# Optimization experiments

Hardware: AMD Instinct MI355X
Metric: run time of the kernel (lower is better)

Reference implementation:

```python
import jax, jax.numpy as jnp
import numpy as np

B, IN, H, O, T = 4096, 128, 1024, 64, 25  # batch, static feat, hidden, outputs, steps


def setup_inputs() -> dict:
    key = jax.random.key(0)
    ks = jax.random.split(key, 11)
    s = 1.0 / np.sqrt(H)  # PyTorch LSTM/Linear uniform init scale
    u = lambda k, sh: jax.random.uniform(k, sh, jnp.float32, -s, s)
    return {
        "static_input": jax.random.normal(ks[0], (B, IN), jnp.float32),
        "W_ih0": u(ks[1], (4 * H, IN + O)),
        "W_hh0": u(ks[2], (4 * H, H)),
        "b_ih0": u(ks[3], (4 * H,)),
        "b_hh0": u(ks[4], (4 * H,)),
        "W_ih1": u(ks[5], (4 * H, H)),
        "W_hh1": u(ks[6], (4 * H, H)),
        "b_ih1": u(ks[7], (4 * H,)),
        "b_hh1": u(ks[8], (4 * H,)),
        "W_out": u(ks[9], (O, H)),
        "b_out": u(ks[10], (O,)),
        "num_steps": T,
    }


def _lstm_cell(x, h, c, W_ih, W_hh, b):
    # PyTorch gate order: input, forget, cell(g), output
    g = x @ W_ih.T + h @ W_hh.T + b
    i, f, gg, o = jnp.split(g, 4, axis=-1)
    c_new = jax.nn.sigmoid(f) * c + jax.nn.sigmoid(i) * jnp.tanh(gg)
    h_new = jax.nn.sigmoid(o) * jnp.tanh(c_new)
    return h_new, c_new


def reference(static_input, W_ih0, W_hh0, b_ih0, b_hh0,
              W_ih1, W_hh1, b_ih1, b_hh1, W_out, b_out, num_steps):
    b0 = b_ih0 + b_hh0
    b1 = b_ih1 + b_hh1
    batch = static_input.shape[0]
    hid = W_hh0.shape[1]
    out_dim = W_out.shape[0]
    z = jnp.zeros((batch, hid), jnp.float32)
    y0 = jnp.zeros((batch, out_dim), jnp.float32)  # output_seq[:, 0] is zeros at t=0

    def step(carry, _):
        h1, c1, h2, c2, y_prev = carry
        x = jnp.concatenate([static_input, y_prev], axis=-1)  # [B, IN+O]
        h1, c1 = _lstm_cell(x, h1, c1, W_ih0, W_hh0, b0)
        h2, c2 = _lstm_cell(h1, h2, c2, W_ih1, W_hh1, b1)
        y = h2 @ W_out.T + b_out  # [B, O]
        return (h1, c1, h2, c2, y), y

    _, ys = jax.lax.scan(step, (z, z, z, z, y0), None, length=num_steps)
    return jnp.transpose(ys, (1, 0, 2))  # [B, T, O]
```

## Files before the change

### kernel.cpp

```cpp
#include <hip/hip_runtime.h>

#define BATCH  4096
#define HID    1024
#define NOUT   64
#define TSTEPS 25
#define KA2    1216
#define KB     2048
#define LDY    1600

typedef __attribute__((ext_vector_type(8))) __bf16 bf16x8;
typedef __attribute__((ext_vector_type(4))) float  floatx4;

__device__ __forceinline__ unsigned short f2bf(float f) {
    union { float f; unsigned u; } v; v.f = f;
    unsigned r = v.u + 0x7fffu + ((v.u >> 16) & 1u);
    return (unsigned short)(r >> 16);
}
__device__ __forceinline__ float rcpf(float x) { return __builtin_amdgcn_rcpf(x); }
__device__ __forceinline__ float sigmf(float x) { return rcpf(1.0f + __expf(-x)); }
__device__ __forceinline__ float tanh_fast(float x) {
    float ax = fabsf(x);
    float e  = __expf(-2.0f * ax);
    float t  = (1.0f - e) * rcpf(1.0f + e);
    return copysignf(t, x);
}

#define GLDS16(gp, lp) __builtin_amdgcn_global_load_lds( \
    (const __attribute__((address_space(1))) void*)(gp), \
    (__attribute__((address_space(3))) void*)(lp), 16, 0, 0)

__global__ __launch_bounds__(1024, 4) void lstm_gate_gemm(
    const unsigned short* __restrict__ X, int K,
    const unsigned short* __restrict__ W,
    const float* __restrict__ ginit,
    float* __restrict__ cell,
    unsigned short* __restrict__ d1, int ld1, int off1,
    unsigned short* __restrict__ d2, int ld2, int off2,
    float* __restrict__ dfp)
{
    __shared__ __align__(16) char smem[65536];

    const int tid  = threadIdx.x;
    const int lane = tid & 63;
    const int w    = tid >> 6;
    const int q    = lane >> 4;
    const int lr   = lane & 15;
    const int wm   = w >> 2;
    const int wn   = w & 3;

    const int id  = blockIdx.y * 16 + blockIdx.x;
    const int xcd = id & 7;
    const int c   = id >> 3;
    const int bx  = (xcd & 3) * 4 + (c & 3);
    const int by  = (xcd >> 2) * 8 + (c >> 2);
    const int m0  = bx * 256;
    const int j0  = by * 64;

    const unsigned short* srcS[2];
    char* ldsS[2];
#pragma unroll
    for (int e = 0; e < 2; ++e) {
        int s = e * 1024 + tid;
        if (s < 1024) {
            int row = s >> 2;
            int kg  = (s & 3) ^ ((row >> 1) & 3);
            srcS[e] = X + (size_t)(m0 + row) * K + kg * 8;
        } else {
            int t   = s - 1024;
            int row = t >> 2;
            int kg  = (t & 3) ^ ((row >> 1) & 3);
            int jj = row >> 2, gate = row & 3;
            srcS[e] = W + (size_t)(gate * HID + j0 + jj) * K + kg * 8;
        }
        ldsS[e] = smem + (size_t)s * 16;
    }

    unsigned offA[4], offB[4];
#pragma unroll
    for (int i = 0; i < 4; ++i) {
        int ra = wm * 64 + i * 16 + lr;
        offA[i] = (unsigned)((ra * 4 + (q ^ ((ra >> 1) & 3))) * 16);
        int rb = wn * 64 + i * 16 + lr;
        offB[i] = (unsigned)(16384 + (rb * 4 + (q ^ ((rb >> 1) & 3))) * 16);
    }

    floatx4 acc[4][4];
#pragma unroll
    for (int i = 0; i < 4; ++i)
#pragma unroll
        for (int j = 0; j < 4; ++j)
            acc[i][j] = floatx4{0.f, 0.f, 0.f, 0.f};

    const int kiters = K >> 5;

#pragma unroll
    for (int e = 0; e < 2; ++e)
        GLDS16(srcS[e], ldsS[e]);

    for (int kt = 0; kt < kiters; ++kt) {
        __syncthreads();
        const int cur = (kt & 1) * 32768;
        if (kt + 1 < kiters) {
            const int koff = (kt + 1) * 32;
            const int nxt  = ((kt + 1) & 1) * 32768;
#pragma unroll
            for (int e = 0; e < 2; ++e)
                GLDS16(srcS[e] + koff, ldsS[e] + nxt);
        }
        bf16x8 av[4], bv[4];
#pragma unroll
        for (int j = 0; j < 4; ++j) bv[j] = *(const bf16x8*)(smem + cur + offB[j]);
#pragma unroll
        for (int i = 0; i < 4; ++i) av[i] = *(const bf16x8*)(smem + cur + offA[i]);
#pragma unroll
        for (int i = 0; i < 4; ++i)
#pragma unroll
            for (int j = 0; j < 4; ++j)
                acc[i][j] = __builtin_amdgcn_mfma_f32_16x16x32_bf16(av[i], bv[j], acc[i][j], 0, 0, 0);
    }

    const int jg = j0 + wn * 16 + lr;
    const float4 gi = *(const float4*)(ginit + (size_t)jg * 4);
    float* scratch = (float*)(void*)smem + w * 1024;

#pragma unroll
    for (int i = 0; i < 4; ++i) {
        __syncthreads();
#pragma unroll
        for (int j = 0; j < 4; ++j)
#pragma unroll
            for (int r = 0; r < 4; ++r)
                scratch[(q * 4 + r) * 64 + j * 16 + lr] = acc[i][j][r];
        __syncthreads();
#pragma unroll
        for (int p = 0; p < 4; ++p) {
            int row = q + p * 4;
            const float4 g = *(const float4*)(scratch + row * 64 + lr * 4);
            int b = m0 + wm * 64 + i * 16 + row;
            float iv = sigmf(g.x + gi.x);
            float fv = sigmf(g.y + gi.y);
            float gv = tanh_fast(g.z + gi.z);
            float ov = sigmf(g.w + gi.w);
            size_t ci = (size_t)b * HID + jg;
            float cn = fv * cell[ci] + iv * gv;
            cell[ci] = cn;
            float hv = ov * tanh_fast(cn);
            unsigned short hb = f2bf(hv);
            d1[(size_t)b * ld1 + off1 + jg] = hb;
            if (d2)  d2[(size_t)b * ld2 + off2 + jg] = hb;
            if (dfp) dfp[(size_t)b * HID + jg] = hv;
        }
    }
}

__global__ __launch_bounds__(256) void out_gemm(
    const float* __restrict__ h2, const float* __restrict__ wt,
    const float* __restrict__ bout, float* __restrict__ y,
    unsigned short* __restrict__ xn)
{
    __shared__ float hl[8 * 1024];
    const int tid = threadIdx.x;
    const int b0 = blockIdx.x * 8;
#pragma unroll
    for (int r = 0; r < 8; ++r) {
        int f4 = r * 256 + tid;
        *(float4*)(hl + f4 * 4) = *(const float4*)(h2 + (size_t)b0 * 1024 + f4 * 4);
    }
    __syncthreads();
    const int o  = tid & 63;
    const int wv = tid >> 6;
    float acc0 = 0.f, acc1 = 0.f;
#pragma unroll 8
    for (int k = 0; k < 1024; ++k) {
        float wvv = wt[k * 64 + o];
        acc0 += hl[(wv * 2 + 0) * 1024 + k] * wvv;
        acc1 += hl[(wv * 2 + 1) * 1024 + k] * wvv;
    }
    float bo = bout[o];
    int b = b0 + wv * 2;
    float y0 = acc0 + bo, y1 = acc1 + bo;
    y[(size_t)b * LDY + o] = y0;
    y[(size_t)(b + 1) * LDY + o] = y1;
    xn[(size_t)b * KA2 + o] = f2bf(y0);
    xn[(size_t)(b + 1) * KA2 + o] = f2bf(y1);
}

__global__ void build_woutT(const float* __restrict__ wout, float* __restrict__ wt)
{
    int idx = blockIdx.x * 256 + threadIdx.x;
    int o = idx & 63, k = idx >> 6;
    wt[idx] = wout[(size_t)o * 1024 + k];
}

__global__ void build_bias(const float* __restrict__ a, const float* __restrict__ b,
                           float* __restrict__ o)
{
    int idx = blockIdx.x * 256 + threadIdx.x;
    int gate = idx & 3, j = idx >> 2;
    int n = gate * 1024 + j;
    o[idx] = a[n] + b[n];
}

__global__ __launch_bounds__(256) void build_w0(
    const float* __restrict__ wih, const float* __restrict__ whh,
    unsigned short* __restrict__ w0)
{
    int idx = blockIdx.x * 256 + threadIdx.x;
    int n = idx / 304;
    int c = (idx - n * 304) * 4;
    float4 v;
    if (c < 64)       v = *(const float4*)(wih + (size_t)n * 192 + 128 + c);
    else if (c < 192) v = *(const float4*)(wih + (size_t)n * 192 + (c - 64));
    else              v = *(const float4*)(whh + (size_t)n * 1024 + (c - 192));
    ushort4 o;
    o.x = f2bf(v.x); o.y = f2bf(v.y); o.z = f2bf(v.z); o.w = f2bf(v.w);
    *(ushort4*)(w0 + (size_t)n * KA2 + c) = o;
}

__global__ __launch_bounds__(256) void build_w1(
    const float* __restrict__ wih, const float* __restrict__ whh,
    unsigned short* __restrict__ w1)
{
    int idx = blockIdx.x * 256 + threadIdx.x;
    int n = idx >> 9;
    int c = (idx & 511) * 4;
    float4 v;
    if (c < 1024) v = *(const float4*)(wih + (size_t)n * 1024 + c);
    else          v = *(const float4*)(whh + (size_t)n * 1024 + (c - 1024));
    ushort4 o;
    o.x = f2bf(v.x); o.y = f2bf(v.y); o.z = f2bf(v.z); o.w = f2bf(v.w);
    *(ushort4*)(w1 + (size_t)n * KB + c) = o;
}

__global__ __launch_bounds__(256) void build_x0static(
    const float* __restrict__ stat, unsigned short* __restrict__ xa,
    unsigned short* __restrict__ xb)
{
    int idx = blockIdx.x * 256 + threadIdx.x;
    int b = idx >> 5;
    int c = (idx & 31) * 4;
    float4 v = *(const float4*)(stat + (size_t)b * 128 + c);
    ushort4 o;
    o.x = f2bf(v.x); o.y = f2bf(v.y); o.z = f2bf(v.z); o.w = f2bf(v.w);
    *(ushort4*)(xa + (size_t)b * KA2 + 64 + c) = o;
    *(ushort4*)(xb + (size_t)b * KA2 + 64 + c) = o;
}

extern "C" void kernel_launch(void* const* d_in, const int* in_sizes, int n_in,
                              void* d_out, int out_size, void* d_ws, size_t ws_size,
                              hipStream_t stream)
{
    (void)in_sizes; (void)n_in; (void)out_size; (void)ws_size;
    const float* static_in = (const float*)d_in[0];
    const float* Wih0 = (const float*)d_in[1];
    const float* Whh0 = (const float*)d_in[2];
    const float* bih0 = (const float*)d_in[3];
    const float* bhh0 = (const float*)d_in[4];
    const float* Wih1 = (const float*)d_in[5];
    const float* Whh1 = (const float*)d_in[6];
    const float* bih1 = (const float*)d_in[7];
    const float* bhh1 = (const float*)d_in[8];
    const float* Wout = (const float*)d_in[9];
    const float* bout = (const float*)d_in[10];
    float* out = (float*)d_out;

    char* p = (char*)d_ws;
    size_t off = 0;
    auto take = [&](size_t n) { char* r = p + off; off += (n + 255) & ~(size_t)255; return r; };

    unsigned short* W0   = (unsigned short*)take((size_t)4096 * KA2 * 2);
    unsigned short* W1   = (unsigned short*)take((size_t)4096 * KB * 2);
    float*          B1b  = (float*)take(4096 * 4);
    float*          B0b  = (float*)take(4096 * 4);
    float*          WoT  = (float*)take((size_t)1024 * 64 * 4);
    float*          H2f  = (float*)take((size_t)BATCH * HID * 4);
    float*          C1   = (float*)take((size_t)BATCH * HID * 4);
    float*          C2   = (float*)take((size_t)BATCH * HID * 4);
    unsigned short* X0a  = (unsigned short*)take((size_t)BATCH * KA2 * 2);
    unsigned short* X0b  = (unsigned short*)take((size_t)BATCH * KA2 * 2);
    unsigned short* X1a  = (unsigned short*)take((size_t)BATCH * KB * 2);
    unsigned short* X1b  = (unsigned short*)take((size_t)BATCH * KB * 2);

    hipMemsetAsync(C1, 0, (size_t)BATCH * HID * 4, stream);
    hipMemsetAsync(C2, 0, (size_t)BATCH * HID * 4, stream);
    hipMemsetAsync(X0a, 0, (size_t)BATCH * KA2 * 2, stream);
    hipMemsetAsync(X0b, 0, (size_t)BATCH * KA2 * 2, stream);
    hipMemsetAsync(X1a, 0, (size_t)BATCH * KB * 2, stream);

    build_w0<<<4864, 256, 0, stream>>>(Wih0, Whh0, W0);
    build_w1<<<8192, 256, 0, stream>>>(Wih1, Whh1, W1);
    build_woutT<<<256, 256, 0, stream>>>(Wout, WoT);
    build_bias<<<16, 256, 0, stream>>>(bih0, bhh0, B0b);
    build_bias<<<16, 256, 0, stream>>>(bih1, bhh1, B1b);
    build_x0static<<<512, 256, 0, stream>>>(static_in, X0a, X0b);

    dim3 grid(16, 16);
    for (int t = 0; t < TSTEPS; ++t) {
        unsigned short* X0c = (t & 1) ? X0b : X0a;
        unsigned short* X0n = (t & 1) ? X0a : X0b;
        unsigned short* X1c = (t & 1) ? X1b : X1a;
        unsigned short* X1n = (t & 1) ? X1a : X1b;
        lstm_gate_gemm<<<grid, 1024, 0, stream>>>(X0c, KA2, W0, B0b, C1,
                                                  X1c, KB, 0, X0n, KA2, 192, nullptr);
        lstm_gate_gemm<<<grid, 1024, 0, stream>>>(X1c, KB, W1, B1b, C2,
                                                  X1n, KB, 1024, nullptr, 0, 0, H2f);
        out_gemm<<<512, 256, 0, stream>>>(H2f, WoT, bout, out + t * NOUT, X0n);
    }
}
```

Before: 3.911 ms.

## Restructure gate GEMM into 8-wave ping-pong pipeline with 64-wide K tiles

Rewrites the LSTM gate GEMM to use 512 threads, 64-deep K tiles, and 128KB of LDS double buffering split into quadrant halves. Loads are staged across four phases per tile, and setprio plus explicit barriers interleave MFMA with global-to-LDS copies. The layer-0 K dimension is padded from 1216 to 1280 with zero weights so it divides evenly by 64. The epilogue is reorganised for the new per-wave tile ownership. This aims to hide memory latency and LDS traffic behind matrix math. In exchange it adds padded work on layer 0, lowers occupancy, and depends on hand-tuned wait counts being correct.

```diff
diff --git a/kernel.cpp b/kernel.cpp
--- a/kernel.cpp
+++ b/kernel.cpp
@@ -4,7 +4,8 @@
 #define HID    1024
 #define NOUT   64
 #define TSTEPS 25
-#define KA2    1216
+#define KA2    1280
+#define KA2R   1216
 #define KB     2048
 #define LDY    1600
 
@@ -29,7 +30,7 @@
     (const __attribute__((address_space(1))) void*)(gp), \
     (__attribute__((address_space(3))) void*)(lp), 16, 0, 0)
 
-__global__ __launch_bounds__(1024, 4) void lstm_gate_gemm(
+__global__ __launch_bounds__(512, 2) void lstm_gate_gemm(
     const unsigned short* __restrict__ X, int K,
     const unsigned short* __restrict__ W,
     const float* __restrict__ ginit,
@@ -38,15 +39,15 @@
     unsigned short* __restrict__ d2, int ld2, int off2,
     float* __restrict__ dfp)
 {
-    __shared__ __align__(16) char smem[65536];
+    __shared__ __align__(16) char smem[131072];
 
     const int tid  = threadIdx.x;
     const int lane = tid & 63;
     const int w    = tid >> 6;
-    const int q    = lane >> 4;
+    const int ql   = lane >> 4;
     const int lr   = lane & 15;
-    const int wm   = w >> 2;
-    const int wn   = w & 3;
+    const int wr   = w >> 2;
+    const int wc   = w & 3;
 
     const int id  = blockIdx.y * 16 + blockIdx.x;
     const int xcd = id & 7;
@@ -56,101 +57,153 @@
     const int m0  = bx * 256;
     const int j0  = by * 64;
 
-    const unsigned short* srcS[2];
-    char* ldsS[2];
-#pragma unroll
-    for (int e = 0; e < 2; ++e) {
-        int s = e * 1024 + tid;
-        if (s < 1024) {
-            int row = s >> 2;
-            int kg  = (s & 3) ^ ((row >> 1) & 3);
-            srcS[e] = X + (size_t)(m0 + row) * K + kg * 8;
-        } else {
-            int t   = s - 1024;
-            int row = t >> 2;
-            int kg  = (t & 3) ^ ((row >> 1) & 3);
-            int jj = row >> 2, gate = row & 3;
-            srcS[e] = W + (size_t)(gate * HID + j0 + jj) * K + kg * 8;
+    const int s0  = w * 128 + lane;
+    const int r0  = s0 >> 3;
+    const int kc0 = (s0 & 7) ^ (r0 & 7);
+    const unsigned sOff = (unsigned)s0 * 16;
+    const unsigned short* sA[2];
+    const unsigned short* sB[2];
+    sA[0] = X + (size_t)(m0 + r0) * K + kc0 * 8;
+    sA[1] = X + (size_t)(m0 + 128 + r0) * K + kc0 * 8;
+    {
+        const int nb0 = r0, nb1 = 128 + r0;
+        sB[0] = W + (size_t)((nb0 & 3) * HID + j0 + (nb0 >> 2)) * K + kc0 * 8;
+        sB[1] = W + (size_t)((nb1 & 3) * HID + j0 + (nb1 >> 2)) * K + kc0 * 8;
+    }
+
+#define STAGE_A(h, tt, p) do { \
+    const unsigned short* _s = sA[h] + (size_t)(tt) * 64; \
+    char* _d = smem + (p) * 65536 + (h) * 16384 + sOff; \
+    GLDS16(_s, _d); \
+    GLDS16(_s + 8 * (size_t)K, _d + 1024); \
+} while (0)
+
+#define STAGE_B(h, tt, p) do { \
+    const unsigned short* _s = sB[h] + (size_t)(tt) * 64; \
+    char* _d = smem + (p) * 65536 + 32768 + (h) * 16384 + sOff; \
+    GLDS16(_s, _d); \
+    GLDS16(_s + 2 * (size_t)K, _d + 1024); \
+} while (0)
+
+    unsigned offA[4], offB[2];
+#pragma unroll
+    for (int fi = 0; fi < 4; ++fi) {
+        int r = wr * 64 + fi * 16 + lr;
+        offA[fi] = (unsigned)((r * 8 + (ql ^ (r & 7))) * 16);
+    }
+#pragma unroll
+    for (int fj = 0; fj < 2; ++fj) {
+        int r = wc * 32 + fj * 16 + lr;
+        offB[fj] = (unsigned)(32768 + (r * 8 + (ql ^ (r & 7))) * 16);
+    }
+
+    floatx4 acc[4][4][2];
+#pragma unroll
+    for (int q = 0; q < 4; ++q)
+#pragma unroll
+        for (int i = 0; i < 4; ++i)
+#pragma unroll
+            for (int j = 0; j < 2; ++j)
+                acc[q][i][j] = floatx4{0.f, 0.f, 0.f, 0.f};
+
+    const int NT = K >> 6;
+
+    STAGE_A(0, 0, 0); STAGE_B(0, 0, 0); STAGE_A(1, 0, 0); STAGE_B(1, 0, 0);
+    STAGE_B(0, 1, 1); STAGE_A(1, 1, 1);
+    asm volatile("s_waitcnt vmcnt(4)");
+    __builtin_amdgcn_s_barrier();
+
+#define PHASE(Q, QA, QB, STG, VM) do { \
+    bf16x8 av[4][2], bv[2][2]; \
+    const char* _ab = smem + cur + (QA) * 16384; \
+    const char* _bb = smem + cur + (QB) * 16384; \
+    _Pragma("unroll") \
+    for (int fj = 0; fj < 2; ++fj) { \
+        bv[fj][0] = *(const bf16x8*)(_bb + offB[fj]); \
+        bv[fj][1] = *(const bf16x8*)(_bb + (offB[fj] ^ 64u)); \
+    } \
+    _Pragma("unroll") \
+    for (int fi = 0; fi < 4; ++fi) { \
+        av[fi][0] = *(const bf16x8*)(_ab + offA[fi]); \
+        av[fi][1] = *(const bf16x8*)(_ab + (offA[fi] ^ 64u)); \
+    } \
+    STG; \
+    VM; \
+    __builtin_amdgcn_s_barrier(); \
+    asm volatile("s_waitcnt lgkmcnt(0)"); \
+    __builtin_amdgcn_sched_barrier(0); \
+    __builtin_amdgcn_s_setprio(1); \
+    _Pragma("unroll") \
+    for (int fi = 0; fi < 4; ++fi) \
+    _Pragma("unroll") \
+    for (int fj = 0; fj < 2; ++fj) \
+    _Pragma("unroll") \
+    for (int kk = 0; kk < 2; ++kk) \
+        acc[Q][fi][fj] = __builtin_amdgcn_mfma_f32_16x16x32_bf16( \
+            av[fi][kk], bv[fj][kk], acc[Q][fi][fj], 0, 0, 0); \
+    __builtin_amdgcn_s_setprio(0); \
+    __builtin_amdgcn_s_barrier(); \
+} while (0)
+
+    int par = 0;
+    for (int t = 0; t < NT; ++t) {
+        const int cur = par * 65536;
+        const int np  = par ^ 1;
+        const int t1  = (t + 1 < NT) ? t + 1 : NT - 1;
+        const int t2  = (t + 2 < NT) ? t + 2 : NT - 1;
+        PHASE(0, 0, 0, STAGE_A(0, t1, np),  (void)0);
+        PHASE(1, 1, 0, STAGE_B(1, t1, np),  (void)0);
+        PHASE(2, 1, 1, STAGE_B(0, t2, par), (void)0);
+        PHASE(3, 0, 1, STAGE_A(1, t2, par), asm volatile("s_waitcnt vmcnt(4)"));
+        par ^= 1;
+    }
+
+    asm volatile("s_waitcnt vmcnt(0)");
+    __builtin_amdgcn_s_barrier();
+
+    float* scratch = (float*)(void*)smem + w * 640;
+    const int jj   = lane & 7;
+    const int rsel = lane >> 3;
+
+#pragma unroll
+    for (int qd = 0; qd < 4; ++qd) {
+        const int qa = (qd == 1 || qd == 2) ? 1 : 0;
+        const int qb = (qd >= 2) ? 1 : 0;
+        const int rowbase = m0 + qa * 128 + wr * 64;
+        const int jg = j0 + qb * 32 + wc * 8 + jj;
+        const float4 gi = *(const float4*)(ginit + (size_t)jg * 4);
+#pragma unroll
+        for (int fi = 0; fi < 4; ++fi) {
+#pragma unroll
+            for (int fj = 0; fj < 2; ++fj)
+#pragma unroll
+                for (int r = 0; r < 4; ++r)
+                    scratch[(ql * 4 + r) * 36 + fj * 16 + lr] = acc[qd][fi][fj][r];
+            asm volatile("" ::: "memory");
+#pragma unroll
+            for (int p = 0; p < 2; ++p) {
+                const int row = rsel + p * 8;
+                const float4 g = *(const float4*)(scratch + row * 36 + jj * 4);
+                const int b = rowbase + fi * 16 + row;
+                float iv = sigmf(g.x + gi.x);
+                float fv = sigmf(g.y + gi.y);
+                float gv = tanh_fast(g.z + gi.z);
+                float ov = sigmf(g.w + gi.w);
+                size_t ci = (size_t)b * HID + jg;
+                float cn = fv * cell[ci] + iv * gv;
+                cell[ci] = cn;
+                float hv = ov * tanh_fast(cn);
+                unsigned short hb = f2bf(hv);
+                d1[(size_t)b * ld1 + off1 + jg] = hb;
+                if (d2)  d2[(size_t)b * ld2 + off2 + jg] = hb;
+                if (dfp) dfp[(size_t)b * HID + jg] = hv;
+            }
+            asm volatile("" ::: "memory");
         }
-        ldsS[e] = smem + (size_t)s * 16;
-    }
-
-    unsigned offA[4], offB[4];
-#pragma unroll
-    for (int i = 0; i < 4; ++i) {
-        int ra = wm * 64 + i * 16 + lr;
-        offA[i] = (unsigned)((ra * 4 + (q ^ ((ra >> 1) & 3))) * 16);
-        int rb = wn * 64 + i * 16 + lr;
-        offB[i] = (unsigned)(16384 + (rb * 4 + (q ^ ((rb >> 1) & 3))) * 16);
-    }
-
-    floatx4 acc[4][4];
-#pragma unroll
-    for (int i = 0; i < 4; ++i)
-#pragma unroll
-        for (int j = 0; j < 4; ++j)
-            acc[i][j] = floatx4{0.f, 0.f, 0.f, 0.f};
-
-    const int kiters = K >> 5;
-
-#pragma unroll
-    for (int e = 0; e < 2; ++e)
-        GLDS16(srcS[e], ldsS[e]);
-
-    for (int kt = 0; kt < kiters; ++kt) {
-        __syncthreads();
-        const int cur = (kt & 1) * 32768;
-        if (kt + 1 < kiters) {
-            const int koff = (kt + 1) * 32;
-            const int nxt  = ((kt + 1) & 1) * 32768;
-#pragma unroll
-            for (int e = 0; e < 2; ++e)
-                GLDS16(srcS[e] + koff, ldsS[e] + nxt);
-        }
-        bf16x8 av[4], bv[4];
-#pragma unroll
-        for (int j = 0; j < 4; ++j) bv[j] = *(const bf16x8*)(smem + cur + offB[j]);
-#pragma unroll
-        for (int i = 0; i < 4; ++i) av[i] = *(const bf16x8*)(smem + cur + offA[i]);
-#pragma unroll
-        for (int i = 0; i < 4; ++i)
-#pragma unroll
-            for (int j = 0; j < 4; ++j)
-                acc[i][j] = __builtin_amdgcn_mfma_f32_16x16x32_bf16(av[i], bv[j], acc[i][j], 0, 0, 0);
-    }
-
-    const int jg = j0 + wn * 16 + lr;
-    const float4 gi = *(const float4*)(ginit + (size_t)jg * 4);
-    float* scratch = (float*)(void*)smem + w * 1024;
-
-#pragma unroll
-    for (int i = 0; i < 4; ++i) {
-        __syncthreads();
-#pragma unroll
-        for (int j = 0; j < 4; ++j)
-#pragma unroll
-            for (int r = 0; r < 4; ++r)
-                scratch[(q * 4 + r) * 64 + j * 16 + lr] = acc[i][j][r];
-        __syncthreads();
-#pragma unroll
-        for (int p = 0; p < 4; ++p) {
-            int row = q + p * 4;
-            const float4 g = *(const float4*)(scratch + row * 64 + lr * 4);
-            int b = m0 + wm * 64 + i * 16 + row;
-            float iv = sigmf(g.x + gi.x);
-            float fv = sigmf(g.y + gi.y);
-            float gv = tanh_fast(g.z + gi.z);
-            float ov = sigmf(g.w + gi.w);
-            size_t ci = (size_t)b * HID + jg;
-            float cn = fv * cell[ci] + iv * gv;
-            cell[ci] = cn;
-            float hv = ov * tanh_fast(cn);
-            unsigned short hb = f2bf(hv);
-            d1[(size_t)b * ld1 + off1 + jg] = hb;
-            if (d2)  d2[(size_t)b * ld2 + off2 + jg] = hb;
-            if (dfp) dfp[(size_t)b * HID + jg] = hv;
-        }
-    }
+    }
+#undef PHASE
+#undef STAGE_A
+#undef STAGE_B
 }
 
 __global__ __launch_bounds__(256) void out_gemm(
@@ -206,12 +259,12 @@
     unsigned short* __restrict__ w0)
 {
     int idx = blockIdx.x * 256 + threadIdx.x;
-    int n = idx / 304;
-    int c = (idx - n * 304) * 4;
-    float4 v;
-    if (c < 64)       v = *(const float4*)(wih + (size_t)n * 192 + 128 + c);
-    else if (c < 192) v = *(const float4*)(wih + (size_t)n * 192 + (c - 64));
-    else              v = *(const float4*)(whh + (size_t)n * 1024 + (c - 192));
+    int n = idx / 320;
+    int c = (idx - n * 320) * 4;
+    float4 v = {0.f, 0.f, 0.f, 0.f};
+    if (c < 64)        v = *(const float4*)(wih + (size_t)n * 192 + 128 + c);
+    else if (c < 192)  v = *(const float4*)(wih + (size_t)n * 192 + (c - 64));
+    else if (c < 1216) v = *(const float4*)(whh + (size_t)n * 1024 + (c - 192));
     ushort4 o;
     o.x = f2bf(v.x); o.y = f2bf(v.y); o.z = f2bf(v.z); o.w = f2bf(v.w);
     *(ushort4*)(w0 + (size_t)n * KA2 + c) = o;
@@ -287,7 +340,7 @@
     hipMemsetAsync(X0b, 0, (size_t)BATCH * KA2 * 2, stream);
     hipMemsetAsync(X1a, 0, (size_t)BATCH * KB * 2, stream);
 
-    build_w0<<<4864, 256, 0, stream>>>(Wih0, Whh0, W0);
+    build_w0<<<5120, 256, 0, stream>>>(Wih0, Whh0, W0);
     build_w1<<<8192, 256, 0, stream>>>(Wih1, Whh1, W1);
     build_woutT<<<256, 256, 0, stream>>>(Wout, WoT);
     build_bias<<<16, 256, 0, stream>>>(bih0, bhh0, B0b);
@@ -300,10 +353,10 @@
         unsigned short* X0n = (t & 1) ? X0a : X0b;
         unsigned short* X1c = (t & 1) ? X1b : X1a;
         unsigned short* X1n = (t & 1) ? X1a : X1b;
-        lstm_gate_gemm<<<grid, 1024, 0, stream>>>(X0c, KA2, W0, B0b, C1,
-                                                  X1c, KB, 0, X0n, KA2, 192, nullptr);
-        lstm_gate_gemm<<<grid, 1024, 0, stream>>>(X1c, KB, W1, B1b, C2,
-                                                  X1n, KB, 1024, nullptr, 0, 0, H2f);
+        lstm_gate_gemm<<<grid, 512, 0, stream>>>(X0c, KA2, W0, B0b, C1,
+                                                 X1c, KB, 0, X0n, KA2, 192, nullptr);
+        lstm_gate_gemm<<<grid, 512, 0, stream>>>(X1c, KB, W1, B1b, C2,
+                                                 X1n, KB, 1024, nullptr, 0, 0, H2f);
         out_gemm<<<512, 256, 0, stream>>>(H2f, WoT, bout, out + t * NOUT, X0n);
     }
 }
```

Result: slower. 4.289 ms (+9.7%).
